# Optimization experiments

Measured on AMD Instinct MI355X. Metric: run time of the kernel, lower is better.

Reference implementation:

```python
import jax, jax.numpy as jnp
import numpy as np

B, T, D = 2, 2048, 2048
H, G = 16, 4          # query heads, kv groups (GQA)
DK = D // H           # 128
THETA = 10000.0


def _rope(x, pos):
    # x: (B, h, T, dk); half-split rotary embedding
    dk = x.shape[-1]
    inv_freq = 1.0 / (THETA ** (jnp.arange(0, dk // 2, dtype=jnp.float32) * 2.0 / dk))
    ang = pos.astype(jnp.float32)[:, None] * inv_freq[None, :]   # (T, dk/2)
    cos, sin = jnp.cos(ang), jnp.sin(ang)                        # (T, dk/2)
    x1, x2 = x[..., : dk // 2], x[..., dk // 2 :]
    return jnp.concatenate([x1 * cos - x2 * sin, x2 * cos + x1 * sin], axis=-1)


def setup_inputs() -> dict:
    key = jax.random.key(0)
    ks = jax.random.split(key, 5)
    scale = D ** -0.5
    x = jax.random.normal(ks[0], (B, T, D), jnp.float32)
    Wq = jax.random.normal(ks[1], (D, H * DK), jnp.float32) * scale
    Wk = jax.random.normal(ks[2], (D, G * DK), jnp.float32) * scale
    Wv = jax.random.normal(ks[3], (D, G * DK), jnp.float32) * scale
    Wo = jax.random.normal(ks[4], (D, D), jnp.float32) * scale
    mask = jnp.tril(jnp.ones((T, T), dtype=bool))   # causal mask, True = attend
    pos = jnp.arange(T, dtype=jnp.int32)
    return {"x": x, "Wq": Wq, "Wk": Wk, "Wv": Wv, "Wo": Wo, "mask": mask, "pos": pos}


def reference(x, Wq, Wk, Wv, Wo, mask, pos):
    b, t, d = x.shape
    # projections (bias-free linears)
    q = (x @ Wq).reshape(b, t, H, DK).transpose(0, 2, 1, 3)   # (b, h, t, dk)
    k = (x @ Wk).reshape(b, t, G, DK).transpose(0, 2, 1, 3)   # (b, g, t, dk)
    v = (x @ Wv).reshape(b, t, G, DK).transpose(0, 2, 1, 3)
    # RoPE on q and k (module applies rope_q(q,q) and rope_k(k,k))
    q = _rope(q, pos)
    k = _rope(k, pos)
    # GQA: repeat_interleave kv heads to match query heads
    rf = H // G
    k = jnp.repeat(k, rf, axis=1)   # (b, h, t, dk)
    v = jnp.repeat(v, rf, axis=1)
    # scores + causal mask + softmax
    att = jnp.einsum('bhtd,bhTd->bhtT', q, k) / np.float32(np.sqrt(DK))
    att = jnp.where(mask[None, None, :, :], att, -jnp.inf)
    att = jax.nn.softmax(att, axis=-1)
    y = jnp.einsum('bhtT,bhTd->bhtd', att, v)
    y = y.transpose(0, 2, 1, 3).reshape(b, t, d)
    return y @ Wo
```

## Files before the change

kernel.cpp:

```cpp
#include <hip/hip_runtime.h>
#include <cstdint>
#include <cmath>


#define GLOBAL_AS __attribute__((address_space(1)))
#define LDS_AS __attribute__((address_space(3)))

typedef __bf16 bf16x8 __attribute__((ext_vector_type(8)));
typedef __bf16 bf16x4 __attribute__((ext_vector_type(4)));
typedef float f32x4 __attribute__((ext_vector_type(4)));
typedef float f32x16 __attribute__((ext_vector_type(16)));

constexpr int Tn = 2048;

__device__ __forceinline__ f32x4 mfma_bf16(bf16x8 a, bf16x8 b, f32x4 c) {
  return __builtin_amdgcn_mfma_f32_16x16x32_bf16(a, b, c, 0, 0, 0);
}
__device__ __forceinline__ f32x16 mfma32(bf16x8 a, bf16x8 b, f32x16 c) {
  return __builtin_amdgcn_mfma_f32_32x32x16_bf16(a, b, c, 0, 0, 0);
}
__device__ __forceinline__ uint32_t pack_bf16(float a, float b) {
  union { __bf16 h[2]; uint32_t u; } c;
  c.h[0] = (__bf16)a;
  c.h[1] = (__bf16)b;
  return c.u;
}

__global__ __launch_bounds__(256) void convert_f32_bf16(const float* __restrict__ src,
                                                        __bf16* __restrict__ dst,
                                                        size_t n4) {
  const size_t i = (size_t)blockIdx.x * 256 + threadIdx.x;
  if (i >= n4) return;
  const f32x4 v = ((const f32x4*)src)[i];
  bf16x4 o;
#pragma unroll
  for (int k = 0; k < 4; ++k) o[k] = (__bf16)v[k];
  ((bf16x4*)dst)[i] = o;
}

__global__ __launch_bounds__(256) void transpose_f32_bf16(const float* __restrict__ src,
                                                          __bf16* __restrict__ dst,
                                                          int K, int N) {
  __shared__ __bf16 tile[32][33];
  const int n0 = blockIdx.x * 32, k0 = blockIdx.y * 32;
  const int tx = threadIdx.x, ty = threadIdx.y;
#pragma unroll
  for (int i = 0; i < 32; i += 8)
    tile[ty + i][tx] = (__bf16)src[(size_t)(k0 + ty + i) * N + n0 + tx];
  __syncthreads();
#pragma unroll
  for (int i = 0; i < 32; i += 8)
    dst[(size_t)(n0 + ty + i) * K + k0 + tx] = tile[tx][ty + i];
}

__global__ __launch_bounds__(256) void transpose_v(const __bf16* __restrict__ qkv,
                                                   __bf16* __restrict__ vtg) {
  __shared__ __bf16 tile[32][33];
  const int bg = blockIdx.z;
  const int b = bg >> 2, g = bg & 3;
  const int key0 = blockIdx.x * 32, d0 = blockIdx.y * 32;
  const int tx = threadIdx.x, ty = threadIdx.y;
  const __bf16* src = qkv + (size_t)b * Tn * 3072 + 2560 + g * 128;
  __bf16* dst = vtg + (size_t)bg * 128 * Tn;
#pragma unroll
  for (int i = 0; i < 32; i += 8)
    tile[ty + i][tx] = src[(size_t)(key0 + ty + i) * 3072 + d0 + tx];
  __syncthreads();
#pragma unroll
  for (int i = 0; i < 32; i += 8)
    dst[(size_t)(d0 + ty + i) * Tn + key0 + tx] = tile[tx][ty + i];
}

__global__ __launch_bounds__(256) void gemm_bt(const __bf16* __restrict__ A,
                                               const __bf16* __restrict__ BT,
                                               void* __restrict__ C,
                                               int K, int ldc, int outf32) {
  __shared__ __attribute__((aligned(16))) __bf16 As[128 * 32];
  __shared__ __attribute__((aligned(16))) __bf16 Bs[128 * 32];
  const int tid = threadIdx.x;
  const int wave = tid >> 6, lane = tid & 63;
  const int lr = lane & 15, lq = lane >> 4;
  const int wm = wave >> 1, wn = wave & 1;
  const int m0 = blockIdx.y * 128, n0 = blockIdx.x * 128;

  f32x4 acc[4][4] = {};

  const int srow = tid >> 2;
  const int scol = (tid & 3) * 8;
  const __bf16* ga = A + (size_t)(m0 + srow) * K + scol;
  const __bf16* gb = BT + (size_t)(n0 + srow) * K + scol;

  for (int kt = 0; kt < K; kt += 32) {
    __syncthreads();
#pragma unroll
    for (int it = 0; it < 2; ++it) {
      __builtin_amdgcn_global_load_lds((GLOBAL_AS void*)(ga + (size_t)it * 64 * K + kt),
                                       (LDS_AS void*)(As + it * 2048 + wave * 512), 16, 0, 0);
      __builtin_amdgcn_global_load_lds((GLOBAL_AS void*)(gb + (size_t)it * 64 * K + kt),
                                       (LDS_AS void*)(Bs + it * 2048 + wave * 512), 16, 0, 0);
    }
    __syncthreads();

    bf16x8 af[4], bfv[4];
#pragma unroll
    for (int i = 0; i < 4; ++i)
      af[i] = *(const bf16x8*)(As + (wm * 64 + i * 16 + lr) * 32 + lq * 8);
#pragma unroll
    for (int j = 0; j < 4; ++j)
      bfv[j] = *(const bf16x8*)(Bs + (wn * 64 + j * 16 + lr) * 32 + lq * 8);
#pragma unroll
    for (int i = 0; i < 4; ++i)
#pragma unroll
      for (int j = 0; j < 4; ++j)
        acc[i][j] = mfma_bf16(af[i], bfv[j], acc[i][j]);
  }

#pragma unroll
  for (int i = 0; i < 4; ++i) {
    const int row = m0 + wm * 64 + i * 16 + lq * 4;
#pragma unroll
    for (int j = 0; j < 4; ++j) {
      const int col = n0 + wn * 64 + j * 16 + lr;
#pragma unroll
      for (int r = 0; r < 4; ++r) {
        if (outf32)
          ((float*)C)[(size_t)(row + r) * ldc + col] = acc[i][j][r];
        else
          ((__bf16*)C)[(size_t)(row + r) * ldc + col] = (__bf16)acc[i][j][r];
      }
    }
  }
}

__global__ __launch_bounds__(256) void rope_kernel(__bf16* __restrict__ qkv) {
  const int row = blockIdx.x;
  const int t = row & (Tn - 1);
  for (int p = threadIdx.x; p < 1280; p += 256) {
    const int d = p & 63;
    const int hh = p >> 6;
    const int col = (hh < 16) ? (hh * 128 + d) : (2048 + (hh - 16) * 128 + d);
    const float inv = exp2f((float)d * (-13.287712379549449f / 64.f));
    const float ang = (float)t * inv;
    float sn, cs;
    __sincosf(ang, &sn, &cs);
    __bf16* ptr = qkv + (size_t)row * 3072 + col;
    const float x1 = (float)ptr[0];
    const float x2 = (float)ptr[64];
    ptr[0] = (__bf16)(x1 * cs - x2 * sn);
    ptr[64] = (__bf16)(x2 * cs + x1 * sn);
  }
}

constexpr int KVB = 64;
__global__ __launch_bounds__(256, 2) void flash_attn(const __bf16* __restrict__ qkv,
                                                     const __bf16* __restrict__ vtg,
                                                     __bf16* __restrict__ y) {
  const int b = blockIdx.y >> 4, h = blockIdx.y & 15;
  const int g = h >> 2;
  const int q0 = ((int)gridDim.x - 1 - (int)blockIdx.x) * 128;
  const int tid = threadIdx.x;
  const int wave = tid >> 6, lane = tid & 63;
  const int l31 = lane & 31, hi = lane >> 5;

  const __bf16* Qb = qkv + (size_t)b * Tn * 3072 + h * 128;
  const __bf16* Kb = qkv + (size_t)b * Tn * 3072 + 2048 + g * 128;
  const __bf16* Vt = vtg + (size_t)(b * 4 + g) * 128 * Tn;

  __shared__ __attribute__((aligned(16))) __bf16 Ks[2][8192];
  __shared__ __attribute__((aligned(16))) __bf16 Vs[2][8192];

  const __bf16* ksrc[4];
  const __bf16* vsrc[4];
#pragma unroll
  for (int i = 0; i < 4; ++i) {
    ksrc[i] = Kb + (size_t)((i >> 1) * 32 + l31) * 3072 + ((i * 4 + wave) & 7) * 16 + hi * 8;
    vsrc[i] = Vt + (size_t)(i * 32 + l31) * Tn + wave * 16 + hi * 8;
  }

  const int qg = q0 + wave * 32 + l31;
  bf16x8 qf[8];
#pragma unroll
  for (int s = 0; s < 8; ++s)
    qf[s] = *(const bf16x8*)(Qb + (size_t)qg * 3072 + s * 16 + hi * 8);

  f32x16 o[4] = {};
  float m_i = -1e30f, l_i = 0.f;
  const float kscale = 0.12752909695983215f;

#pragma unroll
  for (int i = 0; i < 4; ++i) {
    __builtin_amdgcn_global_load_lds((GLOBAL_AS void*)ksrc[i],
                                     (LDS_AS void*)(&Ks[0][(i * 256 + wave * 64) * 8]), 16, 0, 0);
    __builtin_amdgcn_global_load_lds((GLOBAL_AS void*)vsrc[i],
                                     (LDS_AS void*)(&Vs[0][(i * 256 + wave * 64) * 8]), 16, 0, 0);
    ksrc[i] += (size_t)KVB * 3072;
    vsrc[i] += KVB;
  }
  __syncthreads();

  const int ktend = q0 + 128;
  int cur = 0;
  for (int kt = 0; kt < ktend; kt += KVB) {
    if (kt + KVB < ktend) {
#pragma unroll
      for (int i = 0; i < 4; ++i) {
        __builtin_amdgcn_global_load_lds(
            (GLOBAL_AS void*)ksrc[i],
            (LDS_AS void*)(&Ks[cur ^ 1][(i * 256 + wave * 64) * 8]), 16, 0, 0);
        __builtin_amdgcn_global_load_lds(
            (GLOBAL_AS void*)vsrc[i],
            (LDS_AS void*)(&Vs[cur ^ 1][(i * 256 + wave * 64) * 8]), 16, 0, 0);
        ksrc[i] += (size_t)KVB * 3072;
        vsrc[i] += KVB;
      }
    }

    if (kt <= q0 + wave * 32 + 31) {
      f32x16 sa[2] = {};
      __builtin_amdgcn_s_setprio(1);
#pragma unroll
      for (int kb = 0; kb < 2; ++kb)
#pragma unroll
        for (int s = 0; s < 8; ++s) {
          const bf16x8 kf = *(const bf16x8*)(&Ks[cur][((kb * 8 + s) * 64 + lane) * 8]);
          sa[kb] = mfma32(kf, qf[s], sa[kb]);
        }
      __builtin_amdgcn_s_setprio(0);

      const bool full = (kt + KVB - 1) <= (q0 + wave * 32);
      float mx = -1e30f;
      if (full) {
#pragma unroll
        for (int kb = 0; kb < 2; ++kb)
#pragma unroll
          for (int r = 0; r < 16; ++r) {
            const float v = sa[kb][r] * kscale;
            sa[kb][r] = v;
            mx = fmaxf(mx, v);
          }
      } else {
#pragma unroll
        for (int kb = 0; kb < 2; ++kb)
#pragma unroll
          for (int r = 0; r < 16; ++r) {
            const int key = kt + kb * 32 + (r & 3) + 8 * (r >> 2) + 4 * hi;
            const float v = (key <= qg) ? sa[kb][r] * kscale : -1e30f;
            sa[kb][r] = v;
            mx = fmaxf(mx, v);
          }
      }
      mx = fmaxf(mx, __shfl_xor(mx, 32));
      if (__any(mx > m_i + 8.f)) {
        const float mnew = fmaxf(m_i, mx);
        const float alpha = __builtin_amdgcn_exp2f(m_i - mnew);
        m_i = mnew;
        l_i *= alpha;
#pragma unroll
        for (int db = 0; db < 4; ++db)
#pragma unroll
          for (int r = 0; r < 16; ++r) o[db][r] *= alpha;
      }
      float ls = 0.f;
#pragma unroll
      for (int kb = 0; kb < 2; ++kb)
#pragma unroll
        for (int r = 0; r < 16; ++r) {
          const float pv = __builtin_amdgcn_exp2f(sa[kb][r] - m_i);
          sa[kb][r] = pv;
          ls += pv;
        }
      l_i += ls;

      uint32_t P[2][8], X[2][8];
#pragma unroll
      for (int kb = 0; kb < 2; ++kb)
#pragma unroll
        for (int gg = 0; gg < 8; ++gg)
          P[kb][gg] = pack_bf16(sa[kb][2 * gg], sa[kb][2 * gg + 1]);
#pragma unroll
      for (int kb = 0; kb < 2; ++kb)
#pragma unroll
        for (int gg = 0; gg < 8; ++gg)
          X[kb][gg] = (uint32_t)__shfl_xor((int)P[kb][gg], 32);

      union FU { uint32_t u[4]; bf16x8 v; };
      bf16x8 pf[4];
#pragma unroll
      for (int kb = 0; kb < 2; ++kb) {
        FU f0, f1;
        f0.u[0] = hi ? X[kb][2] : P[kb][0];
        f0.u[1] = hi ? X[kb][3] : P[kb][1];
        f0.u[2] = hi ? P[kb][2] : X[kb][0];
        f0.u[3] = hi ? P[kb][3] : X[kb][1];
        f1.u[0] = hi ? X[kb][6] : P[kb][4];
        f1.u[1] = hi ? X[kb][7] : P[kb][5];
        f1.u[2] = hi ? P[kb][6] : X[kb][4];
        f1.u[3] = hi ? P[kb][7] : X[kb][5];
        pf[kb * 2 + 0] = f0.v;
        pf[kb * 2 + 1] = f1.v;
      }

      __builtin_amdgcn_s_setprio(1);
#pragma unroll
      for (int db = 0; db < 4; ++db)
#pragma unroll
        for (int s = 0; s < 4; ++s) {
          const bf16x8 vf = *(const bf16x8*)(&Vs[cur][((db * 4 + s) * 64 + lane) * 8]);
          o[db] = mfma32(vf, pf[s], o[db]);
        }
      __builtin_amdgcn_s_setprio(0);
    }

    __syncthreads();
    cur ^= 1;
  }

  {
    const float lt = l_i + __shfl_xor(l_i, 32);
    const float inv = 1.0f / lt;
    __bf16* yrow = y + (size_t)(b * Tn + qg) * 2048 + h * 128;
#pragma unroll
    for (int db = 0; db < 4; ++db)
#pragma unroll
      for (int g2 = 0; g2 < 4; ++g2) {
        bf16x4 ov;
#pragma unroll
        for (int j = 0; j < 4; ++j) ov[j] = (__bf16)(o[db][4 * g2 + j] * inv);
        *(bf16x4*)(yrow + db * 32 + 8 * g2 + 4 * hi) = ov;
      }
  }
}

extern "C" void kernel_launch(void* const* d_in, const int* in_sizes, int n_in,
                              void* d_out, int out_size, void* d_ws, size_t ws_size,
                              hipStream_t stream) {
  (void)in_sizes; (void)n_in; (void)out_size; (void)ws_size;
  const float* x  = (const float*)d_in[0];
  const float* Wq = (const float*)d_in[1];
  const float* Wk = (const float*)d_in[2];
  const float* Wv = (const float*)d_in[3];
  const float* Wo = (const float*)d_in[4];
  float* out = (float*)d_out;

  __bf16* xb  = (__bf16*)d_ws;
  __bf16* y   = xb;
  __bf16* WT  = xb + (size_t)4096 * 2048;
  __bf16* WoT = WT;
  __bf16* VtG = WT + (size_t)2048 * 2048;
  __bf16* qkv = WT + (size_t)3072 * 2048;

  convert_f32_bf16<<<(4096 * 2048 / 4 + 255) / 256, 256, 0, stream>>>(x, xb, 4096 * 2048 / 4);
  dim3 tb(32, 8);
  transpose_f32_bf16<<<dim3(64, 64), tb, 0, stream>>>(Wq, WT, 2048, 2048);
  transpose_f32_bf16<<<dim3(16, 64), tb, 0, stream>>>(Wk, WT + (size_t)2048 * 2048, 2048, 512);
  transpose_f32_bf16<<<dim3(16, 64), tb, 0, stream>>>(Wv, WT + (size_t)2560 * 2048, 2048, 512);

  gemm_bt<<<dim3(3072 / 128, 4096 / 128), 256, 0, stream>>>(xb, WT, qkv, 2048, 3072, 0);
  rope_kernel<<<4096, 256, 0, stream>>>(qkv);

  transpose_v<<<dim3(Tn / 32, 4, 8), tb, 0, stream>>>(qkv, VtG);
  transpose_f32_bf16<<<dim3(64, 64), tb, 0, stream>>>(Wo, WoT, 2048, 2048);

  flash_attn<<<dim3(Tn / 128, 2 * 16), 256, 0, stream>>>(qkv, VtG, y);
  gemm_bt<<<dim3(2048 / 128, 4096 / 128), 256, 0, stream>>>(y, WoT, out, 2048, 2048, 1);
}
```

Before: 369.8 us.

## Double-buffer GEMM LDS tiles with BK=64 and fragment-ordered layout

The bf16 GEMM now uses two LDS buffers with a K-tile of 64. The next tile is prefetched via global_load_lds while MFMAs run on the current one, so there is one barrier per iteration instead of two. The LDS layout is reordered so each wave reads its MFMA fragments contiguously by lane, which avoids bank conflicts. It also raises MFMA priority with s_setprio and requests occupancy 2, at the cost of 64KB of LDS per block.

```diff
diff --git a/kernel.cpp b/kernel.cpp
--- a/kernel.cpp
+++ b/kernel.cpp
@@ -71,12 +71,12 @@
     dst[(size_t)(d0 + ty + i) * Tn + key0 + tx] = tile[tx][ty + i];
 }
 
-__global__ __launch_bounds__(256) void gemm_bt(const __bf16* __restrict__ A,
-                                               const __bf16* __restrict__ BT,
-                                               void* __restrict__ C,
-                                               int K, int ldc, int outf32) {
-  __shared__ __attribute__((aligned(16))) __bf16 As[128 * 32];
-  __shared__ __attribute__((aligned(16))) __bf16 Bs[128 * 32];
+__global__ __launch_bounds__(256, 2) void gemm_bt(const __bf16* __restrict__ A,
+                                                  const __bf16* __restrict__ BT,
+                                                  void* __restrict__ C,
+                                                  int K, int ldc, int outf32) {
+  __shared__ __attribute__((aligned(16))) __bf16 As[2][8192];
+  __shared__ __attribute__((aligned(16))) __bf16 Bs[2][8192];
   const int tid = threadIdx.x;
   const int wave = tid >> 6, lane = tid & 63;
   const int lr = lane & 15, lq = lane >> 4;
@@ -85,34 +85,64 @@
 
   f32x4 acc[4][4] = {};
 
-  const int srow = tid >> 2;
-  const int scol = (tid & 3) * 8;
-  const __bf16* ga = A + (size_t)(m0 + srow) * K + scol;
-  const __bf16* gb = BT + (size_t)(n0 + srow) * K + scol;
-
-  for (int kt = 0; kt < K; kt += 32) {
+  const __bf16* ga[4];
+  const __bf16* gb[4];
+#pragma unroll
+  for (int j = 0; j < 4; ++j) {
+    const int g = wave * 4 + j;
+    const int row = (g >> 3) * 64 + ((g >> 1) & 3) * 16 + lr;
+    const int col = (g & 1) * 32 + lq * 8;
+    ga[j] = A + (size_t)(m0 + row) * K + col;
+    gb[j] = BT + (size_t)(n0 + row) * K + col;
+  }
+
+#pragma unroll
+  for (int j = 0; j < 4; ++j) {
+    const int g = wave * 4 + j;
+    __builtin_amdgcn_global_load_lds((GLOBAL_AS void*)ga[j],
+                                     (LDS_AS void*)(&As[0][g * 512]), 16, 0, 0);
+    __builtin_amdgcn_global_load_lds((GLOBAL_AS void*)gb[j],
+                                     (LDS_AS void*)(&Bs[0][g * 512]), 16, 0, 0);
+    ga[j] += 64;
+    gb[j] += 64;
+  }
+  __syncthreads();
+
+  int cur = 0;
+  for (int kt = 0; kt < K; kt += 64) {
+    if (kt + 64 < K) {
+#pragma unroll
+      for (int j = 0; j < 4; ++j) {
+        const int g = wave * 4 + j;
+        __builtin_amdgcn_global_load_lds((GLOBAL_AS void*)ga[j],
+                                         (LDS_AS void*)(&As[cur ^ 1][g * 512]), 16, 0, 0);
+        __builtin_amdgcn_global_load_lds((GLOBAL_AS void*)gb[j],
+                                         (LDS_AS void*)(&Bs[cur ^ 1][g * 512]), 16, 0, 0);
+        ga[j] += 64;
+        gb[j] += 64;
+      }
+    }
+
+    bf16x8 af[4][2], bfv[4][2];
+#pragma unroll
+    for (int i = 0; i < 4; ++i)
+#pragma unroll
+      for (int kk = 0; kk < 2; ++kk) {
+        af[i][kk]  = *(const bf16x8*)(&As[cur][((wm * 8 + i * 2 + kk) * 64 + lane) * 8]);
+        bfv[i][kk] = *(const bf16x8*)(&Bs[cur][((wn * 8 + i * 2 + kk) * 64 + lane) * 8]);
+      }
+    __builtin_amdgcn_s_setprio(1);
+#pragma unroll
+    for (int kk = 0; kk < 2; ++kk)
+#pragma unroll
+      for (int i = 0; i < 4; ++i)
+#pragma unroll
+        for (int j = 0; j < 4; ++j)
+          acc[i][j] = mfma_bf16(af[i][kk], bfv[j][kk], acc[i][j]);
+    __builtin_amdgcn_s_setprio(0);
+
     __syncthreads();
-#pragma unroll
-    for (int it = 0; it < 2; ++it) {
-      __builtin_amdgcn_global_load_lds((GLOBAL_AS void*)(ga + (size_t)it * 64 * K + kt),
-                                       (LDS_AS void*)(As + it * 2048 + wave * 512), 16, 0, 0);
-      __builtin_amdgcn_global_load_lds((GLOBAL_AS void*)(gb + (size_t)it * 64 * K + kt),
-                                       (LDS_AS void*)(Bs + it * 2048 + wave * 512), 16, 0, 0);
-    }
-    __syncthreads();
-
-    bf16x8 af[4], bfv[4];
-#pragma unroll
-    for (int i = 0; i < 4; ++i)
-      af[i] = *(const bf16x8*)(As + (wm * 64 + i * 16 + lr) * 32 + lq * 8);
-#pragma unroll
-    for (int j = 0; j < 4; ++j)
-      bfv[j] = *(const bf16x8*)(Bs + (wn * 64 + j * 16 + lr) * 32 + lq * 8);
-#pragma unroll
-    for (int i = 0; i < 4; ++i)
-#pragma unroll
-      for (int j = 0; j < 4; ++j)
-        acc[i][j] = mfma_bf16(af[i], bfv[j], acc[i][j]);
+    cur ^= 1;
   }
 
 #pragma unroll
```

Result: slower. 422.2 us (+14.2%).

## Double-buffer GEMM LDS tiles with fragment-ordered layout and MFMA priority

Applied to the files above, without the earlier changes.

Moves the bf16 GEMM to two LDS buffers per operand, so the next 32-wide K slice is prefetched with global_load_lds while MFMAs run on the current one. This drops one barrier per iteration. The LDS tile is stored in MFMA fragment order, so each lane reads a contiguous 16-byte chunk, which avoids strided bank access. It also raises wave priority around the MFMA block and adds an occupancy hint to launch bounds. The cost is double the LDS use, and the overlap depends on the compiler not inserting a full vmcnt wait before the LDS reads.

```diff
diff --git a/kernel.cpp b/kernel.cpp
--- a/kernel.cpp
+++ b/kernel.cpp
@@ -71,12 +71,12 @@
     dst[(size_t)(d0 + ty + i) * Tn + key0 + tx] = tile[tx][ty + i];
 }
 
-__global__ __launch_bounds__(256) void gemm_bt(const __bf16* __restrict__ A,
-                                               const __bf16* __restrict__ BT,
-                                               void* __restrict__ C,
-                                               int K, int ldc, int outf32) {
-  __shared__ __attribute__((aligned(16))) __bf16 As[128 * 32];
-  __shared__ __attribute__((aligned(16))) __bf16 Bs[128 * 32];
+__global__ __launch_bounds__(256, 5) void gemm_bt(const __bf16* __restrict__ A,
+                                                  const __bf16* __restrict__ BT,
+                                                  void* __restrict__ C,
+                                                  int K, int ldc, int outf32) {
+  __shared__ __attribute__((aligned(16))) __bf16 As[2][4096];
+  __shared__ __attribute__((aligned(16))) __bf16 Bs[2][4096];
   const int tid = threadIdx.x;
   const int wave = tid >> 6, lane = tid & 63;
   const int lr = lane & 15, lq = lane >> 4;
@@ -85,34 +85,56 @@
 
   f32x4 acc[4][4] = {};
 
-  const int srow = tid >> 2;
-  const int scol = (tid & 3) * 8;
-  const __bf16* ga = A + (size_t)(m0 + srow) * K + scol;
-  const __bf16* gb = BT + (size_t)(n0 + srow) * K + scol;
-
+  const __bf16* ga[2];
+  const __bf16* gb[2];
+#pragma unroll
+  for (int jj = 0; jj < 2; ++jj) {
+    const int j = wave * 2 + jj;
+    ga[jj] = A + (size_t)(m0 + j * 16 + lr) * K + lq * 8;
+    gb[jj] = BT + (size_t)(n0 + j * 16 + lr) * K + lq * 8;
+  }
+
+#pragma unroll
+  for (int jj = 0; jj < 2; ++jj) {
+    const int j = wave * 2 + jj;
+    __builtin_amdgcn_global_load_lds((GLOBAL_AS void*)ga[jj],
+                                     (LDS_AS void*)(&As[0][j * 512]), 16, 0, 0);
+    __builtin_amdgcn_global_load_lds((GLOBAL_AS void*)gb[jj],
+                                     (LDS_AS void*)(&Bs[0][j * 512]), 16, 0, 0);
+    ga[jj] += 32;
+    gb[jj] += 32;
+  }
+
+  int cur = 0;
   for (int kt = 0; kt < K; kt += 32) {
     __syncthreads();
-#pragma unroll
-    for (int it = 0; it < 2; ++it) {
-      __builtin_amdgcn_global_load_lds((GLOBAL_AS void*)(ga + (size_t)it * 64 * K + kt),
-                                       (LDS_AS void*)(As + it * 2048 + wave * 512), 16, 0, 0);
-      __builtin_amdgcn_global_load_lds((GLOBAL_AS void*)(gb + (size_t)it * 64 * K + kt),
-                                       (LDS_AS void*)(Bs + it * 2048 + wave * 512), 16, 0, 0);
-    }
-    __syncthreads();
+    if (kt + 32 < K) {
+#pragma unroll
+      for (int jj = 0; jj < 2; ++jj) {
+        const int j = wave * 2 + jj;
+        __builtin_amdgcn_global_load_lds((GLOBAL_AS void*)ga[jj],
+                                         (LDS_AS void*)(&As[cur ^ 1][j * 512]), 16, 0, 0);
+        __builtin_amdgcn_global_load_lds((GLOBAL_AS void*)gb[jj],
+                                         (LDS_AS void*)(&Bs[cur ^ 1][j * 512]), 16, 0, 0);
+        ga[jj] += 32;
+        gb[jj] += 32;
+      }
+    }
 
     bf16x8 af[4], bfv[4];
 #pragma unroll
-    for (int i = 0; i < 4; ++i)
-      af[i] = *(const bf16x8*)(As + (wm * 64 + i * 16 + lr) * 32 + lq * 8);
-#pragma unroll
-    for (int j = 0; j < 4; ++j)
-      bfv[j] = *(const bf16x8*)(Bs + (wn * 64 + j * 16 + lr) * 32 + lq * 8);
+    for (int i = 0; i < 4; ++i) {
+      af[i]  = *(const bf16x8*)(&As[cur][((wm * 4 + i) * 64 + lane) * 8]);
+      bfv[i] = *(const bf16x8*)(&Bs[cur][((wn * 4 + i) * 64 + lane) * 8]);
+    }
+    __builtin_amdgcn_s_setprio(1);
 #pragma unroll
     for (int i = 0; i < 4; ++i)
 #pragma unroll
       for (int j = 0; j < 4; ++j)
         acc[i][j] = mfma_bf16(af[i], bfv[j], acc[i][j]);
+    __builtin_amdgcn_s_setprio(0);
+    cur ^= 1;
   }
 
 #pragma unroll
```

Measured after the change: 535.5 us. 1.45x slower.

## Replace GEMM with 8-wave, 4-stage pipelined kernel using larger tiles

Applied to the files above, without the earlier changes.

Replaces the single-buffered 128x128 bf16 GEMM with a templated 512-thread kernel that uses a 4-deep LDS ring buffer. Global-to-LDS loads are issued three stages ahead, with explicit vmcnt waits and one barrier per k-step, so memory latency overlaps with MFMA work. The QKV projection uses 256x256 tiles and the output projection uses 128x256 tiles. The LDS layout is changed to a fragment-contiguous order, and MFMA sections run at raised wave priority. In exchange, LDS use and register pressure rise, and there are fewer blocks (192 and 256) to fill the CUs.

```diff
diff --git a/kernel.cpp b/kernel.cpp
--- a/kernel.cpp
+++ b/kernel.cpp
@@ -71,59 +71,96 @@
     dst[(size_t)(d0 + ty + i) * Tn + key0 + tx] = tile[tx][ty + i];
 }
 
-__global__ __launch_bounds__(256) void gemm_bt(const __bf16* __restrict__ A,
-                                               const __bf16* __restrict__ BT,
-                                               void* __restrict__ C,
-                                               int K, int ldc, int outf32) {
-  __shared__ __attribute__((aligned(16))) __bf16 As[128 * 32];
-  __shared__ __attribute__((aligned(16))) __bf16 Bs[128 * 32];
+template <int BM, int BN, int OUTF32>
+__global__ __launch_bounds__(512, 2) void gemm8(const __bf16* __restrict__ A,
+                                                const __bf16* __restrict__ BT,
+                                                void* __restrict__ C,
+                                                int K, int ldc) {
+  constexpr int MREP = BM / 32;
+  constexpr int NREP = BN / 64;
+  constexpr int GA = BM / 128;
+  constexpr int GB = BN / 128;
+  constexpr int L = GA + GB;
+  __shared__ __attribute__((aligned(16))) __bf16 As[4][BM * 32];
+  __shared__ __attribute__((aligned(16))) __bf16 Bs[4][BN * 32];
   const int tid = threadIdx.x;
   const int wave = tid >> 6, lane = tid & 63;
   const int lr = lane & 15, lq = lane >> 4;
-  const int wm = wave >> 1, wn = wave & 1;
-  const int m0 = blockIdx.y * 128, n0 = blockIdx.x * 128;
-
-  f32x4 acc[4][4] = {};
-
-  const int srow = tid >> 2;
-  const int scol = (tid & 3) * 8;
-  const __bf16* ga = A + (size_t)(m0 + srow) * K + scol;
-  const __bf16* gb = BT + (size_t)(n0 + srow) * K + scol;
-
-  for (int kt = 0; kt < K; kt += 32) {
-    __syncthreads();
-#pragma unroll
-    for (int it = 0; it < 2; ++it) {
-      __builtin_amdgcn_global_load_lds((GLOBAL_AS void*)(ga + (size_t)it * 64 * K + kt),
-                                       (LDS_AS void*)(As + it * 2048 + wave * 512), 16, 0, 0);
-      __builtin_amdgcn_global_load_lds((GLOBAL_AS void*)(gb + (size_t)it * 64 * K + kt),
-                                       (LDS_AS void*)(Bs + it * 2048 + wave * 512), 16, 0, 0);
-    }
-    __syncthreads();
-
-    bf16x8 af[4], bfv[4];
-#pragma unroll
-    for (int i = 0; i < 4; ++i)
-      af[i] = *(const bf16x8*)(As + (wm * 64 + i * 16 + lr) * 32 + lq * 8);
-#pragma unroll
-    for (int j = 0; j < 4; ++j)
-      bfv[j] = *(const bf16x8*)(Bs + (wn * 64 + j * 16 + lr) * 32 + lq * 8);
-#pragma unroll
-    for (int i = 0; i < 4; ++i)
-#pragma unroll
-      for (int j = 0; j < 4; ++j)
+  const int wm = wave >> 2, wn = wave & 3;
+  const int m0 = blockIdx.y * BM, n0 = blockIdx.x * BN;
+
+  f32x4 acc[MREP][NREP] = {};
+
+  const __bf16* ga[GA];
+  const __bf16* gb[GB];
+#pragma unroll
+  for (int jj = 0; jj < GA; ++jj)
+    ga[jj] = A + (size_t)(m0 + (wave * GA + jj) * 16 + lr) * K + lq * 8;
+#pragma unroll
+  for (int jj = 0; jj < GB; ++jj)
+    gb[jj] = BT + (size_t)(n0 + (wave * GB + jj) * 16 + lr) * K + lq * 8;
+
+  auto stage = [&](int buf) {
+#pragma unroll
+    for (int jj = 0; jj < GA; ++jj) {
+      __builtin_amdgcn_global_load_lds((GLOBAL_AS void*)ga[jj],
+                                       (LDS_AS void*)(&As[buf][(wave * GA + jj) * 512]),
+                                       16, 0, 0);
+      ga[jj] += 32;
+    }
+#pragma unroll
+    for (int jj = 0; jj < GB; ++jj) {
+      __builtin_amdgcn_global_load_lds((GLOBAL_AS void*)gb[jj],
+                                       (LDS_AS void*)(&Bs[buf][(wave * GB + jj) * 512]),
+                                       16, 0, 0);
+      gb[jj] += 32;
+    }
+  };
+
+  stage(0);
+  stage(1);
+  stage(2);
+
+  const int nstep = K >> 5;
+  for (int t = 0; t < nstep; ++t) {
+    if (t + 2 < nstep) {
+      if constexpr (L == 4) asm volatile("s_waitcnt vmcnt(8)" ::: "memory");
+      else                  asm volatile("s_waitcnt vmcnt(6)" ::: "memory");
+    } else if (t + 1 < nstep) {
+      if constexpr (L == 4) asm volatile("s_waitcnt vmcnt(4)" ::: "memory");
+      else                  asm volatile("s_waitcnt vmcnt(3)" ::: "memory");
+    } else {
+      asm volatile("s_waitcnt vmcnt(0)" ::: "memory");
+    }
+    __builtin_amdgcn_s_barrier();
+    if (t + 3 < nstep) stage((t + 3) & 3);
+
+    const int rb = t & 3;
+    bf16x8 af[MREP], bfv[NREP];
+#pragma unroll
+    for (int i = 0; i < MREP; ++i)
+      af[i] = *(const bf16x8*)(&As[rb][((wm * MREP + i) * 64 + lane) * 8]);
+#pragma unroll
+    for (int j = 0; j < NREP; ++j)
+      bfv[j] = *(const bf16x8*)(&Bs[rb][((wn * NREP + j) * 64 + lane) * 8]);
+    __builtin_amdgcn_s_setprio(1);
+#pragma unroll
+    for (int i = 0; i < MREP; ++i)
+#pragma unroll
+      for (int j = 0; j < NREP; ++j)
         acc[i][j] = mfma_bf16(af[i], bfv[j], acc[i][j]);
-  }
-
-#pragma unroll
-  for (int i = 0; i < 4; ++i) {
-    const int row = m0 + wm * 64 + i * 16 + lq * 4;
-#pragma unroll
-    for (int j = 0; j < 4; ++j) {
-      const int col = n0 + wn * 64 + j * 16 + lr;
+    __builtin_amdgcn_s_setprio(0);
+  }
+
+#pragma unroll
+  for (int i = 0; i < MREP; ++i) {
+    const int row = m0 + wm * (MREP * 16) + i * 16 + lq * 4;
+#pragma unroll
+    for (int j = 0; j < NREP; ++j) {
+      const int col = n0 + wn * (NREP * 16) + j * 16 + lr;
 #pragma unroll
       for (int r = 0; r < 4; ++r) {
-        if (outf32)
+        if constexpr (OUTF32)
           ((float*)C)[(size_t)(row + r) * ldc + col] = acc[i][j][r];
         else
           ((__bf16*)C)[(size_t)(row + r) * ldc + col] = (__bf16)acc[i][j][r];
@@ -355,12 +392,12 @@
   transpose_f32_bf16<<<dim3(16, 64), tb, 0, stream>>>(Wk, WT + (size_t)2048 * 2048, 2048, 512);
   transpose_f32_bf16<<<dim3(16, 64), tb, 0, stream>>>(Wv, WT + (size_t)2560 * 2048, 2048, 512);
 
-  gemm_bt<<<dim3(3072 / 128, 4096 / 128), 256, 0, stream>>>(xb, WT, qkv, 2048, 3072, 0);
+  gemm8<256, 256, 0><<<dim3(3072 / 256, 4096 / 256), 512, 0, stream>>>(xb, WT, qkv, 2048, 3072);
   rope_kernel<<<4096, 256, 0, stream>>>(qkv);
 
   transpose_v<<<dim3(Tn / 32, 4, 8), tb, 0, stream>>>(qkv, VtG);
   transpose_f32_bf16<<<dim3(64, 64), tb, 0, stream>>>(Wo, WoT, 2048, 2048);
 
   flash_attn<<<dim3(Tn / 128, 2 * 16), 256, 0, stream>>>(qkv, VtG, y);
-  gemm_bt<<<dim3(2048 / 128, 4096 / 128), 256, 0, stream>>>(y, WoT, out, 2048, 2048, 1);
-}
+  gemm8<128, 256, 1><<<dim3(2048 / 256, 4096 / 128), 512, 0, stream>>>(y, WoT, out, 2048, 2048);
+}
```

Measured after the change: 416.5 us. 1.13x slower.
